# Optimization experiments

Hardware: AMD Instinct MI355X
Metric: run time of the kernel (lower is better)

## Reference

```python
import jax, jax.numpy as jnp
import numpy as np

TEMPERATURE = 0.5
SCALE_LOSS = 1.0 / 32.0
LAMBDA = 0.0039


def setup_inputs() -> dict:
    key = jax.random.key(0)
    z = jax.random.normal(key, (4096, 6, 256), dtype=jnp.float32)
    return {"z": z}


def reference(z):
    B, V = z.shape[0], z.shape[1]
    # [B, V, ...] -> [V, B, D], L2-normalize embeddings
    zv = z.reshape(B, V, -1).transpose(1, 0, 2)
    zn = zv / jnp.linalg.norm(zv, axis=-1, keepdims=True)

    # Positive error: per-sample cross-view similarity [B, V, V]
    sim_pos = jnp.einsum('vbd,wbd->bvw', zn, zn)
    pos = jnp.exp((1.0 - sim_pos) / TEMPERATURE).mean(axis=(1, 2))  # [B]

    # Negative error: per-view within-batch similarity [V, B, B]
    sim_neg = jnp.exp(jnp.einsum('vbd,vcd->vbc', zn, zn) / TEMPERATURE)
    offdiag_mask = ~jnp.eye(B, dtype=bool)  # [B, B]
    off_mean = jnp.where(offdiag_mask[None], sim_neg, 0.0).sum(-1) / (B - 1)  # [V, B]
    neg = off_mean.sum(0)  # [B], accumulated over views

    return jnp.sum(pos) * SCALE_LOSS + LAMBDA * jnp.sum(neg)
```

## Files before the change

### kernel.cpp

```cpp
#include <hip/hip_runtime.h>
#include <cstdint>
#include <cstddef>

#define B_N 4096
#define V_N 6
#define D_N 256
#define CHUNK 8
#define NCHUNK 80
#define NGRAM (NCHUNK * V_N)
#define NPOSB 1024

typedef int i32x4 __attribute__((ext_vector_type(4)));

#define QC 298.0f
#define INV_C2_X2 (2.0f / (QC * QC))

__device__ int g_fin = 0;

__device__ __forceinline__ void async_load16(void* lds, const void* gmem) {
  __builtin_amdgcn_global_load_lds(
      (const __attribute__((address_space(1))) unsigned int*)gmem,
      (__attribute__((address_space(3))) unsigned int*)lds,
      16, 0, 0);
}

__global__ __launch_bounds__(256) void norm_pos_kernel(
    const float* __restrict__ z, signed char* __restrict__ znb,
    float* __restrict__ pos_blk) {
  const int lane = threadIdx.x & 63;
  const int w = threadIdx.x >> 6;
  const int b = blockIdx.x * 4 + w;
  __shared__ float red[4];

  const float4* zb4 = (const float4*)(z + (size_t)b * (V_N * D_N));
  float4 x[V_N];
#pragma unroll
  for (int v = 0; v < V_N; ++v) x[v] = zb4[v * 64 + lane];

  float s[21];
  {
    int p = 0;
#pragma unroll
    for (int v = 0; v < V_N; ++v)
#pragma unroll
      for (int u = v; u < V_N; ++u) {
        s[p] = x[v].x * x[u].x + x[v].y * x[u].y +
               x[v].z * x[u].z + x[v].w * x[u].w;
        ++p;
      }
  }
#pragma unroll
  for (int off = 1; off < 64; off <<= 1)
#pragma unroll
    for (int q = 0; q < 21; ++q)
      s[q] += __shfl_xor(s[q], off);

  const int selfidx[V_N] = {0, 6, 11, 15, 18, 20};
  float inv[V_N];
#pragma unroll
  for (int v = 0; v < V_N; ++v) inv[v] = rsqrtf(s[selfidx[v]]);

#pragma unroll
  for (int v = 0; v < V_N; ++v) {
    const float sc = inv[v] * QC;
    int q0 = (int)rintf(fminf(127.0f, fmaxf(-127.0f, x[v].x * sc)));
    int q1 = (int)rintf(fminf(127.0f, fmaxf(-127.0f, x[v].y * sc)));
    int q2 = (int)rintf(fminf(127.0f, fmaxf(-127.0f, x[v].z * sc)));
    int q3 = (int)rintf(fminf(127.0f, fmaxf(-127.0f, x[v].w * sc)));
    int packed = (q0 & 255) | ((q1 & 255) << 8) | ((q2 & 255) << 16)
               | ((q3 & 255) << 24);
    ((int*)(znb + ((size_t)v * B_N + b) * D_N))[lane] = packed;
  }

  float psum = 0.0f;
  {
    int p = 0;
#pragma unroll
    for (int v = 0; v < V_N; ++v)
#pragma unroll
      for (int u = v; u < V_N; ++u) {
        if (u > v) psum += __expf(2.0f * (1.0f - s[p] * inv[v] * inv[u]));
        ++p;
      }
  }
  if (lane == 0) red[w] = psum;
  __syncthreads();
  if (threadIdx.x == 0)
    pos_blk[blockIdx.x] = red[0] + red[1] + red[2] + red[3];
}

__global__ __launch_bounds__(512, 4) void gram_kernel(
    const signed char* __restrict__ znb, const float* __restrict__ pos_blk,
    float* __restrict__ neg_blk, float* __restrict__ out) {
  const int v = blockIdx.y;
  const int bid = blockIdx.y * NCHUNK + blockIdx.x;

  int i = 31, rem = blockIdx.x;
  for (int r = 31; r >= 0; --r) {
    const int nc = (r + 8) >> 3;
    if (rem < nc) { i = r; break; }
    rem -= nc;
  }
  const int j0 = rem * CHUNK;
  const int jend = min(j0 + CHUNK, i + 1);
  const int nsteps = 2 * (jend - j0);

  const signed char* Zv = znb + (size_t)v * B_N * D_N;
  const signed char* Ag = Zv + (size_t)(i * 128) * D_N;

  __shared__ signed char As[128][256];
  __shared__ signed char Bs[2][128][128];
  __shared__ float red[8];
  __shared__ float pr[8], nr[8];
  __shared__ int lastblk;

  const int tid = threadIdx.x;
  const int lane = tid & 63;
  const int w = tid >> 6;
  const int wr = w >> 2;
  const int wc = w & 3;
  const int kc = lane >> 4;
  const int mrow = wr * 64 + (lane & 15);
  const int ncol = wc * 32 + (lane & 15);

  signed char* AsF = &As[0][0];

#pragma unroll
  for (int q = 0; q < 4; ++q) {
    const int sA = tid + 512 * q;
    const int row = sA >> 4;
    const int gc = (sA & 15) ^ (row & 15);
    async_load16(AsF + sA * 16, Ag + (size_t)row * D_N + gc * 16);
  }
#pragma unroll
  for (int st = 0; st < 2; ++st) {
    if (st < nsteps) {
      const int jn = j0 + (st >> 1), hn = st & 1;
      const signed char* Bg = Zv + (size_t)(jn * 128) * D_N + hn * 128;
      signed char* BsF = &Bs[st & 1][0][0];
#pragma unroll
      for (int q = 0; q < 2; ++q) {
        const int s = tid + 512 * q;
        const int row = s >> 3;
        const int gc = (s & 7) ^ (row & 7);
        async_load16(BsF + s * 16, Bg + (size_t)row * D_N + gc * 16);
      }
    }
  }
  asm volatile("s_waitcnt vmcnt(2)" ::: "memory");
  __builtin_amdgcn_sched_barrier(0);
  __builtin_amdgcn_s_barrier();

  float wsum = 0.0f;
  int s = 0;
  for (int jt = j0; jt < jend; ++jt) {
    i32x4 c[4][2];
#pragma unroll
    for (int a = 0; a < 4; ++a)
#pragma unroll
      for (int b2 = 0; b2 < 2; ++b2) c[a][b2] = (i32x4){0, 0, 0, 0};

#pragma unroll
    for (int h = 0; h < 2; ++h, ++s) {
      const signed char* BsF = &Bs[s & 1][0][0];
      __builtin_amdgcn_s_setprio(1);
#pragma unroll
      for (int kk = 0; kk < 2; ++kk) {
        const int cb8 = kk * 4 + kc;
        const int ca16 = h * 8 + kk * 4 + kc;
        i32x4 af[4], bfr[2];
#pragma unroll
        for (int f = 0; f < 4; ++f) {
          const int ra = mrow + 16 * f;
          af[f] = *(const i32x4*)(AsF + ra * 256 + ((ca16 ^ (ra & 15)) * 16));
        }
#pragma unroll
        for (int f = 0; f < 2; ++f) {
          const int rb = ncol + 16 * f;
          bfr[f] = *(const i32x4*)(BsF + rb * 128 + ((cb8 ^ (rb & 7)) * 16));
        }
#pragma unroll
        for (int fm = 0; fm < 4; ++fm)
#pragma unroll
          for (int fn = 0; fn < 2; ++fn)
            c[fm][fn] = __builtin_amdgcn_mfma_i32_16x16x64_i8(
                af[fm], bfr[fn], c[fm][fn], 0, 0, 0);
      }
      __builtin_amdgcn_s_setprio(0);
      __builtin_amdgcn_s_barrier();
      const int sn = s + 2;
      if (sn < nsteps) {
        const int jn = j0 + (sn >> 1), hn = sn & 1;
        const signed char* Bg = Zv + (size_t)(jn * 128) * D_N + hn * 128;
        signed char* BsN = &Bs[s & 1][0][0];
#pragma unroll
        for (int q = 0; q < 2; ++q) {
          const int sg = tid + 512 * q;
          const int row = sg >> 3;
          const int gc = (sg & 7) ^ (row & 7);
          async_load16(BsN + sg * 16, Bg + (size_t)row * D_N + gc * 16);
        }
      }
      if (h == 1) {
        float tsum = 0.0f;
        if (i != jt) {
#pragma unroll
          for (int fm = 0; fm < 4; ++fm)
#pragma unroll
            for (int fn = 0; fn < 2; ++fn)
#pragma unroll
              for (int r = 0; r < 4; ++r)
                tsum += __expf((float)c[fm][fn][r] * INV_C2_X2);
          wsum += 2.0f * tsum;
        } else {
          const int rb0 = wr * 64 + (lane >> 4) * 4;
          const int cb0 = wc * 32 + (lane & 15);
#pragma unroll
          for (int fm = 0; fm < 4; ++fm)
#pragma unroll
            for (int fn = 0; fn < 2; ++fn) {
              const int gcol = cb0 + fn * 16;
#pragma unroll
              for (int r = 0; r < 4; ++r) {
                const int grow = rb0 + fm * 16 + r;
                float e = __expf((float)c[fm][fn][r] * INV_C2_X2);
                tsum += (grow == gcol) ? 0.0f : e;
              }
            }
          wsum += tsum;
        }
      }
      if (sn < nsteps) {
        asm volatile("s_waitcnt vmcnt(2)" ::: "memory");
      } else {
        asm volatile("s_waitcnt vmcnt(0)" ::: "memory");
      }
      __builtin_amdgcn_sched_barrier(0);
      __builtin_amdgcn_s_barrier();
    }
  }

#pragma unroll
  for (int off = 32; off > 0; off >>= 1) wsum += __shfl_down(wsum, off);
  if (lane == 0) red[w] = wsum;
  __syncthreads();
  if (tid == 0) {
    float bsum = 0.0f;
#pragma unroll
    for (int k = 0; k < 8; ++k) bsum += red[k];
    __hip_atomic_store(&neg_blk[bid], bsum, __ATOMIC_RELAXED,
                       __HIP_MEMORY_SCOPE_AGENT);
    asm volatile("s_waitcnt vmcnt(0)" ::: "memory");
    int t2 = __hip_atomic_fetch_add(&g_fin, 1, __ATOMIC_RELAXED,
                                    __HIP_MEMORY_SCOPE_AGENT);
    lastblk = ((t2 % NGRAM) == NGRAM - 1) ? 1 : 0;
  }
  __syncthreads();

  if (lastblk) {
    float p = 0.0f, n = 0.0f;
    for (int idx = tid; idx < NPOSB; idx += 512) p += pos_blk[idx];
    for (int idx = tid; idx < NGRAM; idx += 512)
      n += __hip_atomic_load(&neg_blk[idx], __ATOMIC_RELAXED,
                             __HIP_MEMORY_SCOPE_AGENT);
#pragma unroll
    for (int off = 32; off > 0; off >>= 1) {
      p += __shfl_down(p, off);
      n += __shfl_down(n, off);
    }
    if (lane == 0) { pr[w] = p; nr[w] = n; }
    __syncthreads();
    if (tid == 0) {
      float P = 0.0f, N = 0.0f;
#pragma unroll
      for (int k = 0; k < 8; ++k) { P += pr[k]; N += nr[k]; }
      out[0] = (1.0f / 32.0f) * ((float)B_N / 6.0f + P / 18.0f) +
               0.0039f * (N / (float)(B_N - 1));
    }
  }
}

extern "C" void kernel_launch(void* const* d_in, const int* in_sizes, int n_in,
                              void* d_out, int out_size, void* d_ws, size_t ws_size,
                              hipStream_t stream) {
  const float* z = (const float*)d_in[0];
  float* out = (float*)d_out;
  float* pos_blk = (float*)d_ws;
  float* neg_blk = (float*)((char*)d_ws + 8192);
  signed char* znb = (signed char*)((char*)d_ws + 32768);

  norm_pos_kernel<<<NPOSB, 256, 0, stream>>>(z, znb, pos_blk);
  dim3 grid(NCHUNK, V_N, 1);
  gram_kernel<<<grid, 512, 0, stream>>>(znb, pos_blk, neg_blk, out);
}
```

Measured before the change: 98.87 us.

## Fuse normalize and gram kernels into one persistent kernel with grid barrier

Merges the normalization/positive-term kernel and the int8 gram kernel into a single launch of 480 blocks. Each block first normalizes and quantizes a slice of rows and accumulates the positive term, then waits at a software grid-wide barrier (atomic counter plus spin) before running its gram tile. This removes one kernel launch and the gap between kernels. In exchange it depends on all 480 blocks being co-resident, which the launch bounds of 4 blocks per CU should allow, and it reduces the first phase's parallelism to 480 blocks.

```diff
diff --git a/kernel.cpp b/kernel.cpp
--- a/kernel.cpp
+++ b/kernel.cpp
@@ -8,13 +8,13 @@
 #define CHUNK 8
 #define NCHUNK 80
 #define NGRAM (NCHUNK * V_N)
-#define NPOSB 1024
 
 typedef int i32x4 __attribute__((ext_vector_type(4)));
 
 #define QC 298.0f
 #define INV_C2_X2 (2.0f / (QC * QC))
 
+__device__ int g_bar = 0;
 __device__ int g_fin = 0;
 
 __device__ __forceinline__ void async_load16(void* lds, const void* gmem) {
@@ -24,78 +24,102 @@
       16, 0, 0);
 }
 
-__global__ __launch_bounds__(256) void norm_pos_kernel(
+__global__ __launch_bounds__(512, 4) void mega_kernel(
     const float* __restrict__ z, signed char* __restrict__ znb,
-    float* __restrict__ pos_blk) {
-  const int lane = threadIdx.x & 63;
-  const int w = threadIdx.x >> 6;
-  const int b = blockIdx.x * 4 + w;
-  __shared__ float red[4];
-
-  const float4* zb4 = (const float4*)(z + (size_t)b * (V_N * D_N));
-  float4 x[V_N];
-#pragma unroll
-  for (int v = 0; v < V_N; ++v) x[v] = zb4[v * 64 + lane];
-
-  float s[21];
+    float* __restrict__ pos_blk, float* __restrict__ neg_blk,
+    float* __restrict__ out) {
+  __shared__ signed char As[128][256];
+  __shared__ signed char Bs[2][128][128];
+  __shared__ float posr[8];
+  __shared__ float red[8];
+  __shared__ float pr[8], nr[8];
+  __shared__ int lastblk;
+
+  const int bx = blockIdx.x;
+  const int tid = threadIdx.x;
+  const int lane = tid & 63;
+  const int w = tid >> 6;
+
+  float pacc = 0.0f;
   {
-    int p = 0;
-#pragma unroll
-    for (int v = 0; v < V_N; ++v)
-#pragma unroll
-      for (int u = v; u < V_N; ++u) {
-        s[p] = x[v].x * x[u].x + x[v].y * x[u].y +
-               x[v].z * x[u].z + x[v].w * x[u].w;
-        ++p;
-      }
-  }
-#pragma unroll
-  for (int off = 1; off < 64; off <<= 1)
-#pragma unroll
-    for (int q = 0; q < 21; ++q)
-      s[q] += __shfl_xor(s[q], off);
-
-  const int selfidx[V_N] = {0, 6, 11, 15, 18, 20};
-  float inv[V_N];
-#pragma unroll
-  for (int v = 0; v < V_N; ++v) inv[v] = rsqrtf(s[selfidx[v]]);
-
-#pragma unroll
-  for (int v = 0; v < V_N; ++v) {
-    const float sc = inv[v] * QC;
-    int q0 = (int)rintf(fminf(127.0f, fmaxf(-127.0f, x[v].x * sc)));
-    int q1 = (int)rintf(fminf(127.0f, fmaxf(-127.0f, x[v].y * sc)));
-    int q2 = (int)rintf(fminf(127.0f, fmaxf(-127.0f, x[v].z * sc)));
-    int q3 = (int)rintf(fminf(127.0f, fmaxf(-127.0f, x[v].w * sc)));
-    int packed = (q0 & 255) | ((q1 & 255) << 8) | ((q2 & 255) << 16)
-               | ((q3 & 255) << 24);
-    ((int*)(znb + ((size_t)v * B_N + b) * D_N))[lane] = packed;
-  }
-
-  float psum = 0.0f;
-  {
-    int p = 0;
-#pragma unroll
-    for (int v = 0; v < V_N; ++v)
-#pragma unroll
-      for (int u = v; u < V_N; ++u) {
-        if (u > v) psum += __expf(2.0f * (1.0f - s[p] * inv[v] * inv[u]));
-        ++p;
-      }
-  }
-  if (lane == 0) red[w] = psum;
+    const int wave_global = bx * 8 + w;
+#pragma unroll
+    for (int rep = 0; rep < 2; ++rep) {
+      if (rep == 1 && wave_global < 3584) break;
+      const int b = (rep == 0) ? wave_global : wave_global + 256;
+
+      const float4* zb4 = (const float4*)(z + (size_t)b * (V_N * D_N));
+      float4 x[V_N];
+#pragma unroll
+      for (int v = 0; v < V_N; ++v) x[v] = zb4[v * 64 + lane];
+
+      float s[21];
+      {
+        int p = 0;
+#pragma unroll
+        for (int v = 0; v < V_N; ++v)
+#pragma unroll
+          for (int u = v; u < V_N; ++u) {
+            s[p] = x[v].x * x[u].x + x[v].y * x[u].y +
+                   x[v].z * x[u].z + x[v].w * x[u].w;
+            ++p;
+          }
+      }
+#pragma unroll
+      for (int off = 1; off < 64; off <<= 1)
+#pragma unroll
+        for (int q = 0; q < 21; ++q)
+          s[q] += __shfl_xor(s[q], off);
+
+      const int selfidx[V_N] = {0, 6, 11, 15, 18, 20};
+      float inv[V_N];
+#pragma unroll
+      for (int v = 0; v < V_N; ++v) inv[v] = rsqrtf(s[selfidx[v]]);
+
+#pragma unroll
+      for (int v = 0; v < V_N; ++v) {
+        const float sc = inv[v] * QC;
+        int q0 = (int)rintf(fminf(127.0f, fmaxf(-127.0f, x[v].x * sc)));
+        int q1 = (int)rintf(fminf(127.0f, fmaxf(-127.0f, x[v].y * sc)));
+        int q2 = (int)rintf(fminf(127.0f, fmaxf(-127.0f, x[v].z * sc)));
+        int q3 = (int)rintf(fminf(127.0f, fmaxf(-127.0f, x[v].w * sc)));
+        int packed = (q0 & 255) | ((q1 & 255) << 8) | ((q2 & 255) << 16)
+                   | ((q3 & 255) << 24);
+        __hip_atomic_store(
+            (int*)(znb + ((size_t)v * B_N + b) * D_N) + lane, packed,
+            __ATOMIC_RELAXED, __HIP_MEMORY_SCOPE_AGENT);
+      }
+
+      {
+        int p = 0;
+#pragma unroll
+        for (int v = 0; v < V_N; ++v)
+#pragma unroll
+          for (int u = v; u < V_N; ++u) {
+            if (u > v) pacc += __expf(2.0f * (1.0f - s[p] * inv[v] * inv[u]));
+            ++p;
+          }
+      }
+    }
+  }
+  if (lane == 0) posr[w] = pacc;
+
+  asm volatile("s_waitcnt vmcnt(0)" ::: "memory");
   __syncthreads();
-  if (threadIdx.x == 0)
-    pos_blk[blockIdx.x] = red[0] + red[1] + red[2] + red[3];
-}
-
-__global__ __launch_bounds__(512, 4) void gram_kernel(
-    const signed char* __restrict__ znb, const float* __restrict__ pos_blk,
-    float* __restrict__ neg_blk, float* __restrict__ out) {
-  const int v = blockIdx.y;
-  const int bid = blockIdx.y * NCHUNK + blockIdx.x;
-
-  int i = 31, rem = blockIdx.x;
+  if (tid == 0) {
+    int t = __hip_atomic_fetch_add(&g_bar, 1, __ATOMIC_RELAXED,
+                                   __HIP_MEMORY_SCOPE_AGENT);
+    const int target = (t / NGRAM + 1) * NGRAM;
+    while (__hip_atomic_load(&g_bar, __ATOMIC_RELAXED,
+                             __HIP_MEMORY_SCOPE_AGENT) < target)
+      __builtin_amdgcn_s_sleep(1);
+  }
+  __syncthreads();
+
+  const int v = bx / NCHUNK;
+  const int cid = bx % NCHUNK;
+
+  int i = 31, rem = cid;
   for (int r = 31; r >= 0; --r) {
     const int nc = (r + 8) >> 3;
     if (rem < nc) { i = r; break; }
@@ -108,15 +132,6 @@
   const signed char* Zv = znb + (size_t)v * B_N * D_N;
   const signed char* Ag = Zv + (size_t)(i * 128) * D_N;
 
-  __shared__ signed char As[128][256];
-  __shared__ signed char Bs[2][128][128];
-  __shared__ float red[8];
-  __shared__ float pr[8], nr[8];
-  __shared__ int lastblk;
-
-  const int tid = threadIdx.x;
-  const int lane = tid & 63;
-  const int w = tid >> 6;
   const int wr = w >> 2;
   const int wc = w & 3;
   const int kc = lane >> 4;
@@ -245,10 +260,12 @@
   if (lane == 0) red[w] = wsum;
   __syncthreads();
   if (tid == 0) {
-    float bsum = 0.0f;
-#pragma unroll
-    for (int k = 0; k < 8; ++k) bsum += red[k];
-    __hip_atomic_store(&neg_blk[bid], bsum, __ATOMIC_RELAXED,
+    float bneg = 0.0f, bpos = 0.0f;
+#pragma unroll
+    for (int k = 0; k < 8; ++k) { bneg += red[k]; bpos += posr[k]; }
+    __hip_atomic_store(&neg_blk[bx], bneg, __ATOMIC_RELAXED,
+                       __HIP_MEMORY_SCOPE_AGENT);
+    __hip_atomic_store(&pos_blk[bx], bpos, __ATOMIC_RELAXED,
                        __HIP_MEMORY_SCOPE_AGENT);
     asm volatile("s_waitcnt vmcnt(0)" ::: "memory");
     int t2 = __hip_atomic_fetch_add(&g_fin, 1, __ATOMIC_RELAXED,
@@ -259,10 +276,12 @@
 
   if (lastblk) {
     float p = 0.0f, n = 0.0f;
-    for (int idx = tid; idx < NPOSB; idx += 512) p += pos_blk[idx];
-    for (int idx = tid; idx < NGRAM; idx += 512)
+    for (int idx = tid; idx < NGRAM; idx += 512) {
+      p += __hip_atomic_load(&pos_blk[idx], __ATOMIC_RELAXED,
+                             __HIP_MEMORY_SCOPE_AGENT);
       n += __hip_atomic_load(&neg_blk[idx], __ATOMIC_RELAXED,
                              __HIP_MEMORY_SCOPE_AGENT);
+    }
 #pragma unroll
     for (int off = 32; off > 0; off >>= 1) {
       p += __shfl_down(p, off);
@@ -289,7 +308,5 @@
   float* neg_blk = (float*)((char*)d_ws + 8192);
   signed char* znb = (signed char*)((char*)d_ws + 32768);
 
-  norm_pos_kernel<<<NPOSB, 256, 0, stream>>>(z, znb, pos_blk);
-  dim3 grid(NCHUNK, V_N, 1);
-  gram_kernel<<<grid, 512, 0, stream>>>(znb, pos_blk, neg_blk, out);
+  mega_kernel<<<NGRAM, 512, 0, stream>>>(z, znb, pos_blk, neg_blk, out);
 }
```

New measurement: 113.0 us. 14.3% more time.
